# Kernel tuning notes

Hardware: AMD Instinct MI355X
Metric: run time of the kernel (lower is better)

The kernel has to match this reference:

```python
import jax, jax.numpy as jnp
import numpy as np

GROUP = 16
LORA_SCALE = 4.0  # lora_alpha(4*r)/r
EPS = 1e-5


def _dequant(q, scale):
    # q: [O, I] int codes in [0,15]; scale: [O, I//GROUP] per-group normalization
    O, I = q.shape
    s = jnp.repeat(scale, GROUP, axis=1)  # [O, I]
    return (q.astype(jnp.float32) / 15.0 * 2.0 - 1.0) * s


def setup_inputs() -> dict:
    key = jax.random.key(0)
    ks = jax.random.split(key, 6)
    B, D, L, R = 16384, 1024, 18, 32
    x = jax.random.normal(ks[0], (B, D), dtype=jnp.float32)
    q_weights = jax.random.randint(ks[1], (L, D, D), 0, 16, dtype=jnp.int32)
    scales = jax.random.uniform(ks[2], (L, D, D // GROUP), dtype=jnp.float32) * 0.05 + 0.005
    biases = jax.random.normal(ks[3], (L, D), dtype=jnp.float32) * 0.02
    lora_a = jax.random.normal(ks[4], (L, R, D), dtype=jnp.float32) * 0.02
    lora_b = jax.random.normal(ks[5], (L, D, R), dtype=jnp.float32) * 0.02
    ln_gamma = jnp.ones((5, D), dtype=jnp.float32)
    ln_beta = jnp.zeros((5, D), dtype=jnp.float32)
    return {"x": x, "q_weights": q_weights, "scales": scales, "biases": biases,
            "lora_a": lora_a, "lora_b": lora_b, "ln_gamma": ln_gamma, "ln_beta": ln_beta}


def _qlora_linear(x, q, scale, bias, la, lb):
    w = _dequant(q, scale)                       # [O, I]
    base = x @ w.T + bias                        # [B, O]
    lora = (x @ la.T) @ lb.T                     # [B, r] -> [B, O]
    return base + LORA_SCALE * lora


def _layernorm(x, g, b):
    mu = jnp.mean(x, axis=-1, keepdims=True)
    var = jnp.mean(jnp.square(x - mu), axis=-1, keepdims=True)
    return (x - mu) * jax.lax.rsqrt(var + EPS) * g + b


def reference(x, q_weights, scales, biases, lora_a, lora_b, ln_gamma, ln_beta):
    h = x
    for blk in range(6):
        r = h
        for j in range(3):
            li = 3 * blk + j
            r = _qlora_linear(r, q_weights[li], scales[li], biases[li], lora_a[li], lora_b[li])
            if j < 2:
                r = jax.nn.relu(r)
        h = r + h  # residual
        if blk < 5:
            h = _layernorm(h, ln_gamma[blk], ln_beta[blk])
    return h
```

## Files before the change

kernel.cpp:

```cpp
#include <hip/hip_runtime.h>
#include <cstdint>
#include <cstddef>

#define D 1024
#define BATCH 16384
#define NLAYERS 18
#define RR 32

typedef __attribute__((ext_vector_type(8))) __bf16 bf16x8;
typedef __attribute__((ext_vector_type(4))) float f32x4;
typedef __attribute__((address_space(3))) void lds_void_t;
typedef __attribute__((address_space(1))) void gmem_void_t;

__device__ __forceinline__ unsigned short f2bf(float f) {
    unsigned int b = __builtin_bit_cast(unsigned int, f);
    b += 0x7fffu + ((b >> 16) & 1u);
    return (unsigned short)(b >> 16);
}
__device__ __forceinline__ float bf2f(unsigned short u) {
    return __builtin_bit_cast(float, (unsigned int)u << 16);
}

__global__ __launch_bounds__(256) void prep_weights(
    const int* __restrict__ q, const float* __restrict__ scales,
    const float* __restrict__ la, const float* __restrict__ lb,
    unsigned short* __restrict__ weff) {
    __shared__ float la_s[32][260];
    __shared__ float lb_s[64][33];
    const int b = blockIdx.x;
    const int li = b >> 6;
    const int o0 = ((b >> 2) & 15) << 6;
    const int i0 = (b & 3) << 8;
    const int t = threadIdx.x;

    {
        const float* src = lb + ((size_t)li * D + o0) * RR;
        for (int i = t; i < 512; i += 256) {
            float4 v = ((const float4*)src)[i];
            const int o = i >> 3, c = (i & 7) << 2;
            lb_s[o][c] = v.x; lb_s[o][c + 1] = v.y; lb_s[o][c + 2] = v.z; lb_s[o][c + 3] = v.w;
        }
    }
    {
        for (int i = t; i < 2048; i += 256) {
            const int r = i >> 6, c = (i & 63) << 2;
            float4 v = *(const float4*)(la + ((size_t)li * RR + r) * D + i0 + c);
            la_s[r][c] = v.x; la_s[r][c + 1] = v.y; la_s[r][c + 2] = v.z; la_s[r][c + 3] = v.w;
        }
    }
    __syncthreads();

    for (int cidx = t; cidx < 2048; cidx += 256) {
        const int ol = cidx >> 5;
        const int i8 = (cidx & 31) << 3;
        float acc[8] = {0.f, 0.f, 0.f, 0.f, 0.f, 0.f, 0.f, 0.f};
#pragma unroll 8
        for (int r = 0; r < 32; ++r) {
            const float bv = lb_s[ol][r];
#pragma unroll
            for (int j = 0; j < 8; ++j) acc[j] += bv * la_s[r][i8 + j];
        }
        const size_t row = (size_t)li * D + o0 + ol;
        const int col = i0 + i8;
        const float s = scales[row * (D / 16) + (col >> 4)];
        const int* qp = q + row * D + col;
        int4 q0 = ((const int4*)qp)[0], q1 = ((const int4*)qp)[1];
        int qa[8] = {q0.x, q0.y, q0.z, q0.w, q1.x, q1.y, q1.z, q1.w};
        union { unsigned short us[8]; int4 v; } u;
        const float c = 2.0f / 15.0f;
#pragma unroll
        for (int j = 0; j < 8; ++j)
            u.us[j] = f2bf(((float)qa[j] * c - 1.0f) * s + 4.0f * acc[j]);
        *(int4*)(weff + row * D + col) = u.v;
    }
}

__global__ __launch_bounds__(256) void init_h(const float* __restrict__ x,
                                              float* __restrict__ h,
                                              unsigned short* __restrict__ xb) {
    const size_t i = (size_t)blockIdx.x * 256 + threadIdx.x;
    float4 v = ((const float4*)x)[i];
    ((float4*)h)[i] = v;
    ushort4 u;
    u.x = f2bf(v.x); u.y = f2bf(v.y); u.z = f2bf(v.z); u.w = f2bf(v.w);
    ((ushort4*)xb)[i] = u;
}

#define BAR_PRE()  asm volatile("s_waitcnt vmcnt(12)" ::: "memory")
#define SBAR() do { asm volatile("" ::: "memory"); __builtin_amdgcn_s_barrier(); asm volatile("" ::: "memory"); } while (0)

__global__ __launch_bounds__(512, 2) void gemm256(
    const unsigned short* __restrict__ xb, const unsigned short* __restrict__ w,
    const float* __restrict__ bias,
    unsigned short* __restrict__ outb, int mode) {
    __shared__ __align__(16) char smem[131072];
    const int tid = threadIdx.x;
    const int wid = tid >> 6, lane = tid & 63;
    const int m0 = blockIdx.y << 8;
    const int n0 = blockIdx.x << 8;
    const int l15 = lane & 15, kgrp = lane >> 4;
    const int wrow = (wid >> 2) << 7;
    const int wcol = (wid & 3) << 6;

    f32x4 acc[8][4];
#pragma unroll
    for (int i = 0; i < 8; ++i)
#pragma unroll
        for (int j = 0; j < 4; ++j) acc[i][j] = 0.0f;

#define STAGE(hs)                                                              \
    do {                                                                       \
        const int slot_ = (hs) & 3;                                            \
        const int k0_ = (hs) << 5;                                             \
        char* sA_ = smem + slot_ * 32768;                                      \
        _Pragma("unroll")                                                      \
        for (int i_ = 0; i_ < 2; ++i_) {                                       \
            const int off_ = i_ * 8192 + (tid << 4);                           \
            const int r_ = off_ >> 6;                                          \
            const int j_ = ((off_ >> 4) & 3) ^ ((r_ >> 1) & 3);                \
            const unsigned short* ga_ = xb + (size_t)(m0 + r_) * D + k0_ + (j_ << 3); \
            const unsigned short* gb_ = w + (size_t)(n0 + r_) * D + k0_ + (j_ << 3);  \
            char* lA_ = sA_ + i_ * 8192 + (wid << 10);                         \
            __builtin_amdgcn_global_load_lds((const gmem_void_t*)ga_, (lds_void_t*)lA_, 16, 0, 0);          \
            __builtin_amdgcn_global_load_lds((const gmem_void_t*)gb_, (lds_void_t*)(lA_ + 16384), 16, 0, 0); \
        }                                                                      \
    } while (0)

#define COMPUTE(hs)                                                            \
    do {                                                                       \
        const char* sA_ = smem + ((hs) & 3) * 32768;                           \
        const char* sB_ = sA_ + 16384;                                         \
        bf16x8 a_[8], b_[4];                                                   \
        _Pragma("unroll")                                                      \
        for (int f_ = 0; f_ < 8; ++f_) {                                       \
            const int r_ = wrow + (f_ << 4) + l15;                             \
            a_[f_] = *(const bf16x8*)(sA_ + (r_ << 6) + ((kgrp ^ ((r_ >> 1) & 3)) << 4)); \
        }                                                                      \
        _Pragma("unroll")                                                      \
        for (int g_ = 0; g_ < 4; ++g_) {                                       \
            const int r_ = wcol + (g_ << 4) + l15;                             \
            b_[g_] = *(const bf16x8*)(sB_ + (r_ << 6) + ((kgrp ^ ((r_ >> 1) & 3)) << 4)); \
        }                                                                      \
        __builtin_amdgcn_s_setprio(1);                                         \
        _Pragma("unroll")                                                      \
        for (int mi_ = 0; mi_ < 8; ++mi_)                                      \
            _Pragma("unroll")                                                  \
            for (int ni_ = 0; ni_ < 4; ++ni_)                                  \
                acc[mi_][ni_] = __builtin_amdgcn_mfma_f32_16x16x32_bf16(       \
                    a_[mi_], b_[ni_], acc[mi_][ni_], 0, 0, 0);                 \
        __builtin_amdgcn_s_setprio(0);                                         \
    } while (0)

    STAGE(0); STAGE(1); STAGE(2);
    for (int h = 0; h < 29; ++h) {
        STAGE(h + 3);
        BAR_PRE();
        SBAR();
        COMPUTE(h);
        SBAR();
    }
    asm volatile("s_waitcnt vmcnt(8)" ::: "memory");
    SBAR(); COMPUTE(29); SBAR();
    asm volatile("s_waitcnt vmcnt(4)" ::: "memory");
    SBAR(); COMPUTE(30); SBAR();
    asm volatile("s_waitcnt vmcnt(0)" ::: "memory");
    SBAR(); COMPUTE(31);

    const int crow = kgrp << 2;
    float bv[4];
#pragma unroll
    for (int ni = 0; ni < 4; ++ni) bv[ni] = bias[n0 + wcol + (ni << 4) + l15];
#pragma unroll
    for (int mi = 0; mi < 8; ++mi) {
        const int rbase = m0 + wrow + (mi << 4) + crow;
#pragma unroll
        for (int ni = 0; ni < 4; ++ni) {
            const int col = n0 + wcol + (ni << 4) + l15;
#pragma unroll
            for (int r = 0; r < 4; ++r) {
                float v = acc[mi][ni][r] + bv[ni];
                if (mode == 0) v = v > 0.0f ? v : 0.0f;
                outb[(size_t)(rbase + r) * D + col] = f2bf(v);
            }
        }
    }
}

__global__ __launch_bounds__(256) void resid_ln_v(
    float* __restrict__ h, const unsigned short* __restrict__ vb,
    unsigned short* __restrict__ xb,
    const float* __restrict__ gamma, const float* __restrict__ beta) {
    const int row = blockIdx.x;
    const int t = threadIdx.x;
    float* hr = h + (size_t)row * D;
    float4 v = ((float4*)hr)[t];
    ushort4 vv = ((const ushort4*)(vb + (size_t)row * D))[t];
    v.x += bf2f(vv.x); v.y += bf2f(vv.y); v.z += bf2f(vv.z); v.w += bf2f(vv.w);
    float s = v.x + v.y + v.z + v.w;
    float s2 = v.x * v.x + v.y * v.y + v.z * v.z + v.w * v.w;
#pragma unroll
    for (int off = 32; off > 0; off >>= 1) {
        s += __shfl_down(s, off);
        s2 += __shfl_down(s2, off);
    }
    __shared__ float red[8];
    const int wid = t >> 6, lane = t & 63;
    if (lane == 0) { red[wid] = s; red[wid + 4] = s2; }
    __syncthreads();
    s = red[0] + red[1] + red[2] + red[3];
    s2 = red[4] + red[5] + red[6] + red[7];
    const float mu = s * (1.0f / D);
    const float var = s2 * (1.0f / D) - mu * mu;
    const float rs = rsqrtf(var + 1e-5f);
    float4 g = ((const float4*)gamma)[t];
    float4 b = ((const float4*)beta)[t];
    float4 o;
    o.x = (v.x - mu) * rs * g.x + b.x;
    o.y = (v.y - mu) * rs * g.y + b.y;
    o.z = (v.z - mu) * rs * g.z + b.z;
    o.w = (v.w - mu) * rs * g.w + b.w;
    ((float4*)hr)[t] = o;
    ushort4 u;
    u.x = f2bf(o.x); u.y = f2bf(o.y); u.z = f2bf(o.z); u.w = f2bf(o.w);
    ((ushort4*)(xb + (size_t)row * D))[t] = u;
}

__global__ __launch_bounds__(256) void final_add(
    const float* __restrict__ h, const unsigned short* __restrict__ vb,
    float* __restrict__ out) {
    const size_t i = (size_t)blockIdx.x * 256 + threadIdx.x;
    float4 hv = ((const float4*)h)[i];
    ushort4 vv = ((const ushort4*)vb)[i];
    float4 o;
    o.x = hv.x + bf2f(vv.x); o.y = hv.y + bf2f(vv.y);
    o.z = hv.z + bf2f(vv.z); o.w = hv.w + bf2f(vv.w);
    ((float4*)out)[i] = o;
}

extern "C" void kernel_launch(void* const* d_in, const int* in_sizes, int n_in,
                              void* d_out, int out_size, void* d_ws, size_t ws_size,
                              hipStream_t stream) {
    const float* x      = (const float*)d_in[0];
    const int*   q      = (const int*)d_in[1];
    const float* scales = (const float*)d_in[2];
    const float* biases = (const float*)d_in[3];
    const float* la     = (const float*)d_in[4];
    const float* lb     = (const float*)d_in[5];
    const float* lng    = (const float*)d_in[6];
    const float* lnb    = (const float*)d_in[7];
    float* out = (float*)d_out;

    char* p = (char*)d_ws;
    unsigned short* weff = (unsigned short*)p; p += (size_t)NLAYERS * D * D * 2;
    unsigned short* xbA  = (unsigned short*)p; p += (size_t)BATCH * D * 2;
    unsigned short* xbB  = (unsigned short*)p; p += (size_t)BATCH * D * 2;
    float*          h    = (float*)p;

    prep_weights<<<NLAYERS * 16 * 4, 256, 0, stream>>>(q, scales, la, lb, weff);
    init_h<<<BATCH * D / 4 / 256, 256, 0, stream>>>(x, h, xbA);

    dim3 ggrid(D / 256, BATCH / 256);
    for (int blk = 0; blk < 6; ++blk) {
        const int li = 3 * blk;
        gemm256<<<ggrid, 512, 0, stream>>>(xbA, weff + (size_t)li * D * D,
                                           biases + (size_t)li * D, xbB, 0);
        gemm256<<<ggrid, 512, 0, stream>>>(xbB, weff + (size_t)(li + 1) * D * D,
                                           biases + (size_t)(li + 1) * D, xbA, 0);
        gemm256<<<ggrid, 512, 0, stream>>>(xbA, weff + (size_t)(li + 2) * D * D,
                                           biases + (size_t)(li + 2) * D, xbB, 1);
        if (blk < 5)
            resid_ln_v<<<BATCH, 256, 0, stream>>>(h, xbB, xbA,
                                                  lng + (size_t)blk * D, lnb + (size_t)blk * D);
        else
            final_add<<<BATCH * D / 4 / 256, 256, 0, stream>>>(h, xbB, out);
    }
}
```

Measured before the change: 973.6 us.

## Split GEMM k-step into two half-phases, remap blocks per XCD, stage weight-prep stores

The GEMM main loop is restructured so each k-step loads and computes half the A fragments at a time, with the global-to-LDS prefetch split into two halves interleaved between the MFMA phases and extra barriers. This is meant to overlap memory and compute more finely and lower register pressure. Block indices are remapped so consecutive M tiles land on the same XCD, sharing weight and activation tiles in that XCD's L2. The weight-prep kernel keeps LoRA B in registers, vectorizes its LDS reads, and stages output through LDS for coalesced stores. The extra barriers per k-step may add synchronization overhead.

```diff
diff --git a/kernel.cpp b/kernel.cpp
--- a/kernel.cpp
+++ b/kernel.cpp
@@ -27,6 +27,7 @@
     unsigned short* __restrict__ weff) {
     __shared__ float la_s[32][260];
     __shared__ float lb_s[64][33];
+    __shared__ unsigned short out_s[64][264];
     const int b = blockIdx.x;
     const int li = b >> 6;
     const int o0 = ((b >> 2) & 15) << 6;
@@ -50,29 +51,45 @@
     }
     __syncthreads();
 
-    for (int cidx = t; cidx < 2048; cidx += 256) {
-        const int ol = cidx >> 5;
-        const int i8 = (cidx & 31) << 3;
+    const int ol = t & 63;
+    const int ibase = (t >> 6) << 6;
+    const size_t grow = (size_t)li * D + o0 + ol;
+    float lbr[32];
+#pragma unroll
+    for (int r = 0; r < 32; ++r) lbr[r] = lb_s[ol][r];
+
+#pragma unroll 1
+    for (int iter = 0; iter < 8; ++iter) {
+        const int i8 = ibase + (iter << 3);
+        const int col = i0 + i8;
+        const float s = scales[grow * (D / 16) + (col >> 4)];
+        const int* qp = q + grow * D + col;
+        int4 q0 = ((const int4*)qp)[0], q1 = ((const int4*)qp)[1];
+
         float acc[8] = {0.f, 0.f, 0.f, 0.f, 0.f, 0.f, 0.f, 0.f};
-#pragma unroll 8
+#pragma unroll 16
         for (int r = 0; r < 32; ++r) {
-            const float bv = lb_s[ol][r];
-#pragma unroll
-            for (int j = 0; j < 8; ++j) acc[j] += bv * la_s[r][i8 + j];
-        }
-        const size_t row = (size_t)li * D + o0 + ol;
-        const int col = i0 + i8;
-        const float s = scales[row * (D / 16) + (col >> 4)];
-        const int* qp = q + row * D + col;
-        int4 q0 = ((const int4*)qp)[0], q1 = ((const int4*)qp)[1];
+            float4 u0 = *(const float4*)&la_s[r][i8];
+            float4 u1 = *(const float4*)&la_s[r][i8 + 4];
+            const float bv = lbr[r];
+            acc[0] += bv * u0.x; acc[1] += bv * u0.y; acc[2] += bv * u0.z; acc[3] += bv * u0.w;
+            acc[4] += bv * u1.x; acc[5] += bv * u1.y; acc[6] += bv * u1.z; acc[7] += bv * u1.w;
+        }
         int qa[8] = {q0.x, q0.y, q0.z, q0.w, q1.x, q1.y, q1.z, q1.w};
         union { unsigned short us[8]; int4 v; } u;
         const float c = 2.0f / 15.0f;
 #pragma unroll
         for (int j = 0; j < 8; ++j)
             u.us[j] = f2bf(((float)qa[j] * c - 1.0f) * s + 4.0f * acc[j]);
-        *(int4*)(weff + row * D + col) = u.v;
-    }
+        *(int4*)&out_s[ol][i8] = u.v;
+    }
+    __syncthreads();
+
+    const int row = t >> 2, cg = (t & 3) << 6;
+    const size_t gbase = ((size_t)li * D + o0 + row) * D + i0 + cg;
+#pragma unroll
+    for (int j = 0; j < 8; ++j)
+        *(int4*)(weff + gbase + (j << 3)) = *(const int4*)&out_s[row][cg + (j << 3)];
 }
 
 __global__ __launch_bounds__(256) void init_h(const float* __restrict__ x,
@@ -86,7 +103,6 @@
     ((ushort4*)xb)[i] = u;
 }
 
-#define BAR_PRE()  asm volatile("s_waitcnt vmcnt(12)" ::: "memory")
 #define SBAR() do { asm volatile("" ::: "memory"); __builtin_amdgcn_s_barrier(); asm volatile("" ::: "memory"); } while (0)
 
 __global__ __launch_bounds__(512, 2) void gemm256(
@@ -96,8 +112,10 @@
     __shared__ __align__(16) char smem[131072];
     const int tid = threadIdx.x;
     const int wid = tid >> 6, lane = tid & 63;
-    const int m0 = blockIdx.y << 8;
-    const int n0 = blockIdx.x << 8;
+    const int bid = blockIdx.x + (blockIdx.y << 2);
+    const int xcd = bid & 7, slot = bid >> 3;
+    const int m0 = ((xcd << 3) + (slot >> 2)) << 8;
+    const int n0 = (slot & 3) << 8;
     const int l15 = lane & 15, kgrp = lane >> 4;
     const int wrow = (wid >> 2) << 7;
     const int wcol = (wid & 3) << 6;
@@ -108,63 +126,77 @@
 #pragma unroll
         for (int j = 0; j < 4; ++j) acc[i][j] = 0.0f;
 
-#define STAGE(hs)                                                              \
+#define STAGE_HALF(hs, i_)                                                     \
     do {                                                                       \
-        const int slot_ = (hs) & 3;                                            \
         const int k0_ = (hs) << 5;                                             \
-        char* sA_ = smem + slot_ * 32768;                                      \
-        _Pragma("unroll")                                                      \
-        for (int i_ = 0; i_ < 2; ++i_) {                                       \
-            const int off_ = i_ * 8192 + (tid << 4);                           \
-            const int r_ = off_ >> 6;                                          \
-            const int j_ = ((off_ >> 4) & 3) ^ ((r_ >> 1) & 3);                \
-            const unsigned short* ga_ = xb + (size_t)(m0 + r_) * D + k0_ + (j_ << 3); \
-            const unsigned short* gb_ = w + (size_t)(n0 + r_) * D + k0_ + (j_ << 3);  \
-            char* lA_ = sA_ + i_ * 8192 + (wid << 10);                         \
-            __builtin_amdgcn_global_load_lds((const gmem_void_t*)ga_, (lds_void_t*)lA_, 16, 0, 0);          \
-            __builtin_amdgcn_global_load_lds((const gmem_void_t*)gb_, (lds_void_t*)(lA_ + 16384), 16, 0, 0); \
-        }                                                                      \
+        char* sA_ = smem + ((hs) & 3) * 32768;                                 \
+        const int off_ = (i_) * 8192 + (tid << 4);                             \
+        const int r_ = off_ >> 6;                                              \
+        const int j_ = ((off_ >> 4) & 3) ^ ((r_ >> 1) & 3);                    \
+        const unsigned short* ga_ = xb + (size_t)(m0 + r_) * D + k0_ + (j_ << 3); \
+        const unsigned short* gb_ = w + (size_t)(n0 + r_) * D + k0_ + (j_ << 3);  \
+        char* lA_ = sA_ + (i_) * 8192 + (wid << 10);                           \
+        __builtin_amdgcn_global_load_lds((const gmem_void_t*)ga_, (lds_void_t*)lA_, 16, 0, 0);          \
+        __builtin_amdgcn_global_load_lds((const gmem_void_t*)gb_, (lds_void_t*)(lA_ + 16384), 16, 0, 0); \
     } while (0)
 
-#define COMPUTE(hs)                                                            \
-    do {                                                                       \
-        const char* sA_ = smem + ((hs) & 3) * 32768;                           \
-        const char* sB_ = sA_ + 16384;                                         \
-        bf16x8 a_[8], b_[4];                                                   \
-        _Pragma("unroll")                                                      \
-        for (int f_ = 0; f_ < 8; ++f_) {                                       \
-            const int r_ = wrow + (f_ << 4) + l15;                             \
-            a_[f_] = *(const bf16x8*)(sA_ + (r_ << 6) + ((kgrp ^ ((r_ >> 1) & 3)) << 4)); \
-        }                                                                      \
-        _Pragma("unroll")                                                      \
-        for (int g_ = 0; g_ < 4; ++g_) {                                       \
-            const int r_ = wcol + (g_ << 4) + l15;                             \
-            b_[g_] = *(const bf16x8*)(sB_ + (r_ << 6) + ((kgrp ^ ((r_ >> 1) & 3)) << 4)); \
-        }                                                                      \
-        __builtin_amdgcn_s_setprio(1);                                         \
-        _Pragma("unroll")                                                      \
-        for (int mi_ = 0; mi_ < 8; ++mi_)                                      \
-            _Pragma("unroll")                                                  \
-            for (int ni_ = 0; ni_ < 4; ++ni_)                                  \
-                acc[mi_][ni_] = __builtin_amdgcn_mfma_f32_16x16x32_bf16(       \
-                    a_[mi_], b_[ni_], acc[mi_][ni_], 0, 0, 0);                 \
-        __builtin_amdgcn_s_setprio(0);                                         \
-    } while (0)
-
-    STAGE(0); STAGE(1); STAGE(2);
-    for (int h = 0; h < 29; ++h) {
-        STAGE(h + 3);
-        BAR_PRE();
+    STAGE_HALF(0, 0); STAGE_HALF(0, 1);
+    STAGE_HALF(1, 0); STAGE_HALF(1, 1);
+    STAGE_HALF(2, 0); STAGE_HALF(2, 1);
+    asm volatile("s_waitcnt vmcnt(8)" ::: "memory");
+    SBAR();
+
+    for (int h = 0; h < 32; ++h) {
+        const char* sA = smem + (h & 3) * 32768;
+        const char* sB = sA + 16384;
+        bf16x8 a[8], b[4];
+#pragma unroll
+        for (int f = 0; f < 4; ++f) {
+            const int r = wrow + (f << 4) + l15;
+            a[f] = *(const bf16x8*)(sA + (r << 6) + ((kgrp ^ ((r >> 1) & 3)) << 4));
+        }
+#pragma unroll
+        for (int g = 0; g < 4; ++g) {
+            const int r = wcol + (g << 4) + l15;
+            b[g] = *(const bf16x8*)(sB + (r << 6) + ((kgrp ^ ((r >> 1) & 3)) << 4));
+        }
+        if (h < 29) STAGE_HALF(h + 3, 0);
         SBAR();
-        COMPUTE(h);
+        asm volatile("s_waitcnt lgkmcnt(0)" ::: "memory");
+        __builtin_amdgcn_s_setprio(1);
+#pragma unroll
+        for (int mi = 0; mi < 4; ++mi)
+#pragma unroll
+            for (int ni = 0; ni < 4; ++ni)
+                acc[mi][ni] = __builtin_amdgcn_mfma_f32_16x16x32_bf16(
+                    a[mi], b[ni], acc[mi][ni], 0, 0, 0);
+        __builtin_amdgcn_s_setprio(0);
         SBAR();
-    }
-    asm volatile("s_waitcnt vmcnt(8)" ::: "memory");
-    SBAR(); COMPUTE(29); SBAR();
-    asm volatile("s_waitcnt vmcnt(4)" ::: "memory");
-    SBAR(); COMPUTE(30); SBAR();
-    asm volatile("s_waitcnt vmcnt(0)" ::: "memory");
-    SBAR(); COMPUTE(31);
+#pragma unroll
+        for (int f = 4; f < 8; ++f) {
+            const int r = wrow + (f << 4) + l15;
+            a[f] = *(const bf16x8*)(sA + (r << 6) + ((kgrp ^ ((r >> 1) & 3)) << 4));
+        }
+        if (h < 29) {
+            STAGE_HALF(h + 3, 1);
+            asm volatile("s_waitcnt vmcnt(8)" ::: "memory");
+        } else if (h == 29) {
+            asm volatile("s_waitcnt vmcnt(4)" ::: "memory");
+        } else if (h == 30) {
+            asm volatile("s_waitcnt vmcnt(0)" ::: "memory");
+        }
+        SBAR();
+        asm volatile("s_waitcnt lgkmcnt(0)" ::: "memory");
+        __builtin_amdgcn_s_setprio(1);
+#pragma unroll
+        for (int mi = 4; mi < 8; ++mi)
+#pragma unroll
+            for (int ni = 0; ni < 4; ++ni)
+                acc[mi][ni] = __builtin_amdgcn_mfma_f32_16x16x32_bf16(
+                    a[mi], b[ni], acc[mi][ni], 0, 0, 0);
+        __builtin_amdgcn_s_setprio(0);
+        SBAR();
+    }
 
     const int crow = kgrp << 2;
     float bv[4];
```

Measured after the change: 940.2 us. -3.4%, faster.
